# Kernel tuning notes

Measured on AMD Instinct MI355X. Metric: run time of the kernel, lower is better.

## Reference

```python
import jax, jax.numpy as jnp
import numpy as np

NUM_EXPERT = 16
IN_DIM = 1024
OUT_DIM = 3072
TOTAL_TOKENS = 16384  # tokens pre-grouped by expert, contiguous blocks


def setup_inputs() -> dict:
    key = jax.random.key(0)
    k1, k2, k3 = jax.random.split(key, 3)
    inp = jax.random.normal(k1, (TOTAL_TOKENS, IN_DIM), dtype=jnp.float32)
    # per-expert token counts (sum == TOTAL_TOKENS); even split here
    fwd_expert_count = jnp.full((NUM_EXPERT,), TOTAL_TOKENS // NUM_EXPERT, dtype=jnp.int64)
    scale = 1.0 / np.sqrt(IN_DIM)
    weight = jax.random.normal(k2, (NUM_EXPERT, OUT_DIM, IN_DIM), dtype=jnp.float32) * scale
    bias = jax.random.normal(k3, (NUM_EXPERT, OUT_DIM), dtype=jnp.float32) * scale
    return {"inp": inp, "fwd_expert_count": fwd_expert_count, "weight": weight, "bias": bias}


def reference(inp, fwd_expert_count, weight, bias):
    # Grouped GEMM: token block e (size fwd_expert_count[e]) uses expert e's
    # weight: y = x @ W_e^T + b_e.  Tokens are contiguous per expert, so
    # expert id per token = repeat(arange(E), counts).
    T = inp.shape[0]
    E = weight.shape[0]
    expert_id = jnp.repeat(jnp.arange(E), fwd_expert_count, total_repeat_length=T)  # [T]
    out = jnp.zeros((T, weight.shape[1]), dtype=inp.dtype)
    # small fixed structural loop over experts (E=16); each iter is a dense GEMM
    for e in range(E):
        ye = inp @ weight[e].T + bias[e]  # [T, out_dim]
        out = jnp.where((expert_id == e)[:, None], ye, out)
    return out
```

## Files before the change

### kernel.cpp

```cpp
#include <hip/hip_runtime.h>

typedef __attribute__((ext_vector_type(8)))  _Float16 f16x8;
typedef __attribute__((ext_vector_type(2)))  __fp16   fp16x2;
typedef __attribute__((ext_vector_type(4)))  float    f32x4;

#define TT 16384
#define KD 1024
#define ND 3072
#define NE 16
#define ASZ (TT * KD)
#define WSZ (NE * ND * KD)
#define NEED_WS ((size_t)(ASZ + WSZ) * 2)

#define BM 256
#define BN 256
#define BK 64
#define NSTEP (KD / BK)
#define ROWB (BK * 2)

#define BAR() __builtin_amdgcn_s_barrier()
#define WAIT_VM(n) asm volatile("s_waitcnt vmcnt(" #n ")" ::: "memory")

__device__ __forceinline__ int swz(int row, int kbyte) {
    return row * ROWB + (kbyte ^ ((row & 7) << 4));
}

__device__ __forceinline__ int find_expert(const void* cntp, int row0) {
    const int* w = (const int*)cntp;
    int oddsum = 0;
    #pragma unroll
    for (int i = 1; i < 16; i += 2) oddsum |= w[i];
    int e = 0;
    long long cum = 0;
    if (oddsum == 0) {
        const long long* c = (const long long*)cntp;
        #pragma unroll
        for (int i = 0; i < NE; ++i) { if ((long long)row0 >= cum) e = i; cum += c[i]; }
    } else {
        #pragma unroll
        for (int i = 0; i < NE; ++i) { if ((long long)row0 >= cum) e = i; cum += w[i]; }
    }
    return e;
}

__device__ __forceinline__ void gl16(const void* g, void* l) {
    __builtin_amdgcn_global_load_lds(
        (const __attribute__((address_space(1))) unsigned int*)g,
        (__attribute__((address_space(3))) unsigned int*)l, 16, 0, 0);
}

__global__ __launch_bounds__(256) void cvt_kernel(const float* __restrict__ A,
                                                  const float* __restrict__ W,
                                                  _Float16* __restrict__ dst) {
    size_t i = ((size_t)blockIdx.x * 256 + threadIdx.x) * 8;
    const float* src = (i < (size_t)ASZ) ? (A + i) : (W + (i - ASZ));
    f32x4 v0 = *(const f32x4*)src;
    f32x4 v1 = *(const f32x4*)(src + 4);
    f16x8 h;
    h[0] = (_Float16)v0[0]; h[1] = (_Float16)v0[1];
    h[2] = (_Float16)v0[2]; h[3] = (_Float16)v0[3];
    h[4] = (_Float16)v1[0]; h[5] = (_Float16)v1[1];
    h[6] = (_Float16)v1[2]; h[7] = (_Float16)v1[3];
    *(f16x8*)(dst + i) = h;
}

#define MFMA_Q(MH, NH) do {                                                  \
    _Pragma("unroll")                                                        \
    for (int kk = 0; kk < 2; ++kk)                                           \
        _Pragma("unroll")                                                    \
        for (int m = 0; m < 4; ++m)                                          \
            _Pragma("unroll")                                                \
            for (int n = 0; n < 2; ++n)                                      \
                acc[MH][NH][m][n] = __builtin_amdgcn_mfma_f32_16x16x32_f16(  \
                    af[kk][m], bf[kk][n], acc[MH][NH][m][n], 0, 0, 0);       \
} while (0)

__launch_bounds__(512, 2)
__global__ void gemm16(const _Float16* __restrict__ A16,
                       const void* __restrict__ cnt,
                       const _Float16* __restrict__ W16,
                       const float* __restrict__ bias,
                       float* __restrict__ Y) {
    __shared__ __align__(16) char Aslot[2][2][128 * ROWB];
    __shared__ __align__(16) char Bslot[2][2][128 * ROWB];

    const int nwg = gridDim.x;
    const int bid0 = blockIdx.x;
    const int wgid = (bid0 & 7) * (nwg >> 3) + (bid0 >> 3);

    const int mt = wgid / (ND / BN);
    const int nt = wgid % (ND / BN);
    const int row0 = mt * BM;
    const int col0 = nt * BN;

    const int e = find_expert(cnt, row0);
    const _Float16* We = W16 + (size_t)e * ND * KD;

    const int tid = threadIdx.x;
    const int l = tid & 63;
    const int w = tid >> 6;
    const int wr = w >> 2;
    const int wc = w & 3;
    const int lr = l & 15;
    const int lk = l >> 4;

    const int laneoff = ((l & 7) * 16) ^ ((l >> 3) << 4);
    const size_t srcoff = (size_t)(w * 16 + (l >> 3)) * (KD * 2) + laneoff;

    const char* gA0 = (const char*)A16 + (size_t)row0 * (KD * 2);
    const char* gA1 = gA0 + (size_t)128 * (KD * 2);
    const char* gB0 = (const char*)We + (size_t)col0 * (KD * 2);
    const char* gB1 = gB0 + (size_t)128 * (KD * 2);

    auto stage_half = [&](const char* ghalf, char* slot, int t) {
        const char* s = ghalf + t * 128 + srcoff;
        gl16(s,                slot + w * 2048);
        gl16(s + 8 * (KD * 2), slot + w * 2048 + 1024);
    };

    f32x4 acc[2][2][4][2] = {};

    stage_half(gA0, &Aslot[0][0][0], 0);
    stage_half(gB0, &Bslot[0][0][0], 0);
    stage_half(gA1, &Aslot[1][0][0], 0);
    stage_half(gB1, &Bslot[1][0][0], 0);
    stage_half(gA0, &Aslot[0][1][0], 1);
    stage_half(gB0, &Bslot[0][1][0], 1);
    WAIT_VM(4);
    BAR();

    for (int t = 0; t < NSTEP; ++t) {
        const int par = t & 1, nxt = par ^ 1;
        const char* A0s = Aslot[0][par];
        const char* A1s = Aslot[1][par];
        const char* B0s = Bslot[0][par];
        const char* B1s = Bslot[1][par];

        f16x8 af[2][4], bf[2][2];

        auto read_A = [&](const char* slot) {
            #pragma unroll
            for (int kk = 0; kk < 2; ++kk)
                #pragma unroll
                for (int m = 0; m < 4; ++m) {
                    int r = wr * 64 + m * 16 + lr;
                    af[kk][m] = *(const f16x8*)&slot[swz(r, kk * 64 + lk * 16)];
                }
        };
        auto read_B = [&](const char* slot) {
            #pragma unroll
            for (int kk = 0; kk < 2; ++kk)
                #pragma unroll
                for (int n = 0; n < 2; ++n) {
                    int r = wc * 32 + n * 16 + lr;
                    bf[kk][n] = *(const f16x8*)&slot[swz(r, kk * 64 + lk * 16)];
                }
        };

        read_A(A0s);
        read_B(B0s);
        if (t + 1 < NSTEP) {
            stage_half(gA1, &Aslot[1][nxt][0], t + 1);
            stage_half(gB1, &Bslot[1][nxt][0], t + 1);
        }
        BAR();
        __builtin_amdgcn_s_setprio(1);
        MFMA_Q(0, 0);
        __builtin_amdgcn_s_setprio(0);
        BAR();

        read_B(B1s);
        if (t + 2 < NSTEP) stage_half(gA0, &Aslot[0][par][0], t + 2);
        BAR();
        __builtin_amdgcn_s_setprio(1);
        MFMA_Q(0, 1);
        __builtin_amdgcn_s_setprio(0);
        BAR();

        read_A(A1s);
        read_B(B0s);
        BAR();
        __builtin_amdgcn_s_setprio(1);
        MFMA_Q(1, 0);
        __builtin_amdgcn_s_setprio(0);
        BAR();

        read_B(B1s);
        if (t + 2 < NSTEP) stage_half(gB0, &Bslot[0][par][0], t + 2);
        BAR();
        __builtin_amdgcn_s_setprio(1);
        MFMA_Q(1, 1);
        __builtin_amdgcn_s_setprio(0);
        if (t + 2 < NSTEP) { WAIT_VM(4); }
        else if (t + 1 < NSTEP) { WAIT_VM(0); }
        BAR();
    }

    float bv[2][2];
    #pragma unroll
    for (int nh = 0; nh < 2; ++nh)
        #pragma unroll
        for (int n = 0; n < 2; ++n)
            bv[nh][n] = bias[(size_t)e * ND + col0 + nh * 128 + wc * 32 + n * 16 + lr];
    #pragma unroll
    for (int mh = 0; mh < 2; ++mh)
        #pragma unroll
        for (int nh = 0; nh < 2; ++nh)
            #pragma unroll
            for (int m = 0; m < 4; ++m)
                #pragma unroll
                for (int j = 0; j < 4; ++j) {
                    int r = row0 + mh * 128 + wr * 64 + m * 16 + lk * 4 + j;
                    float* yp = Y + (size_t)r * ND + col0 + nh * 128 + wc * 32 + lr;
                    yp[0]  = acc[mh][nh][m][0][j] + bv[nh][0];
                    yp[16] = acc[mh][nh][m][1][j] + bv[nh][1];
                }
}

__launch_bounds__(512, 2)
__global__ void fallback_gemm(const float* __restrict__ A,
                              const void* __restrict__ cnt,
                              const float* __restrict__ W,
                              const float* __restrict__ bias,
                              float* __restrict__ Y) {
    __shared__ __align__(16) char ldsbuf[2][2][BM * ROWB];

    const int nwg = gridDim.x;
    const int bid0 = blockIdx.x;
    const int wgid = (bid0 & 7) * (nwg >> 3) + (bid0 >> 3);

    const int mt = wgid / (ND / BN);
    const int nt = wgid % (ND / BN);
    const int row0 = mt * BM;
    const int col0 = nt * BN;

    const int e = find_expert(cnt, row0);
    const float* We = W + (size_t)e * ND * KD;

    const int tid = threadIdx.x;
    const int lane = tid & 63;
    const int w = tid >> 6;
    const int wr = w >> 2;
    const int wc = w & 3;
    const int lr = lane & 15;
    const int lk = lane >> 4;

    int soff[4];
    size_t aoff[4], boff[4];
    #pragma unroll
    for (int c = 0; c < 4; ++c) {
        int q = c * 512 + tid;
        int r = q >> 3;
        int kb = (q & 7) * 8;
        soff[c] = swz(r, kb * 2);
        aoff[c] = (size_t)(row0 + r) * KD + kb;
        boff[c] = (size_t)(col0 + r) * KD + kb;
    }

    f32x4 ra[4][2], rb[4][2];

    auto load_regs = [&](int ks) {
        const int k0 = ks * BK;
        #pragma unroll
        for (int c = 0; c < 4; ++c) {
            const float* ap = A + aoff[c] + k0;
            ra[c][0] = *(const f32x4*)ap;
            ra[c][1] = *(const f32x4*)(ap + 4);
            const float* bp = We + boff[c] + k0;
            rb[c][0] = *(const f32x4*)bp;
            rb[c][1] = *(const f32x4*)(bp + 4);
        }
    };

    auto write_lds = [&](int buf) {
        #pragma unroll
        for (int c = 0; c < 4; ++c) {
            union { f16x8 v; fp16x2 h[4]; } ua, ub;
            ua.h[0] = __builtin_amdgcn_cvt_pkrtz(ra[c][0][0], ra[c][0][1]);
            ua.h[1] = __builtin_amdgcn_cvt_pkrtz(ra[c][0][2], ra[c][0][3]);
            ua.h[2] = __builtin_amdgcn_cvt_pkrtz(ra[c][1][0], ra[c][1][1]);
            ua.h[3] = __builtin_amdgcn_cvt_pkrtz(ra[c][1][2], ra[c][1][3]);
            ub.h[0] = __builtin_amdgcn_cvt_pkrtz(rb[c][0][0], rb[c][0][1]);
            ub.h[1] = __builtin_amdgcn_cvt_pkrtz(rb[c][0][2], rb[c][0][3]);
            ub.h[2] = __builtin_amdgcn_cvt_pkrtz(rb[c][1][0], rb[c][1][1]);
            ub.h[3] = __builtin_amdgcn_cvt_pkrtz(rb[c][1][2], rb[c][1][3]);
            *(f16x8*)&ldsbuf[buf][0][soff[c]] = ua.v;
            *(f16x8*)&ldsbuf[buf][1][soff[c]] = ub.v;
        }
    };

    f32x4 acc[8][4] = {};

    auto compute = [&](const char* Asb, const char* Bsb) {
        #pragma unroll
        for (int kk = 0; kk < 2; ++kk) {
            f16x8 af[8], bf[4];
            #pragma unroll
            for (int m = 0; m < 8; ++m) {
                int r = wr * 128 + m * 16 + lr;
                af[m] = *(const f16x8*)&Asb[swz(r, kk * 64 + lk * 16)];
            }
            #pragma unroll
            for (int n = 0; n < 4; ++n) {
                int r = wc * 64 + n * 16 + lr;
                bf[n] = *(const f16x8*)&Bsb[swz(r, kk * 64 + lk * 16)];
            }
            #pragma unroll
            for (int m = 0; m < 8; ++m)
                #pragma unroll
                for (int n = 0; n < 4; ++n)
                    acc[m][n] = __builtin_amdgcn_mfma_f32_16x16x32_f16(
                        af[m], bf[n], acc[m][n], 0, 0, 0);
        }
    };

    load_regs(0);
    write_lds(0);
    __syncthreads();

    for (int t = 0; t < NSTEP; ++t) {
        const int buf = t & 1;
        if (t + 1 < NSTEP) load_regs(t + 1);
        compute(ldsbuf[buf][0], ldsbuf[buf][1]);
        __syncthreads();
        if (t + 1 < NSTEP) write_lds(buf ^ 1);
        __syncthreads();
    }

    const int cb = col0 + wc * 64;
    const int rb0_ = row0 + wr * 128;
    float bv[4];
    #pragma unroll
    for (int n = 0; n < 4; ++n) bv[n] = bias[(size_t)e * ND + cb + n * 16 + lr];
    #pragma unroll
    for (int m = 0; m < 8; ++m) {
        #pragma unroll
        for (int j = 0; j < 4; ++j) {
            int r = rb0_ + m * 16 + lk * 4 + j;
            float* yp = Y + (size_t)r * ND + cb + lr;
            #pragma unroll
            for (int n = 0; n < 4; ++n)
                yp[n * 16] = acc[m][n][j] + bv[n];
        }
    }
}

extern "C" void kernel_launch(void* const* d_in, const int* in_sizes, int n_in,
                              void* d_out, int out_size, void* d_ws, size_t ws_size,
                              hipStream_t stream) {
    const float* inp  = (const float*)d_in[0];
    const void*  cnt  = d_in[1];
    const float* wgt  = (const float*)d_in[2];
    const float* bias = (const float*)d_in[3];
    float* out = (float*)d_out;

    dim3 grid((TT / BM) * (ND / BN));
    dim3 block(512);

    if (ws_size >= NEED_WS) {
        _Float16* ws16 = (_Float16*)d_ws;
        cvt_kernel<<<dim3((ASZ + WSZ) / (8 * 256)), dim3(256), 0, stream>>>(inp, wgt, ws16);
        gemm16<<<grid, block, 0, stream>>>(ws16, cnt, ws16 + ASZ, bias, out);
    } else {
        fallback_gemm<<<grid, block, 0, stream>>>(inp, cnt, wgt, bias, out);
    }
}
```

Measured before the change: 224.0 us.

## Restructure GEMM main loop with register fragment reuse and fewer barriers

Result: faster. 197.0 us (-12.0%).

```diff
diff --git a/kernel.cpp b/kernel.cpp
--- a/kernel.cpp
+++ b/kernel.cpp
@@ -64,7 +64,8 @@
     *(f16x8*)(dst + i) = h;
 }
 
-#define MFMA_Q(MH, NH) do {                                                  \
+#define MFMA16(AF, BF, MH, NH) do {                                          \
+    __builtin_amdgcn_s_setprio(1);                                           \
     _Pragma("unroll")                                                        \
     for (int kk = 0; kk < 2; ++kk)                                           \
         _Pragma("unroll")                                                    \
@@ -72,7 +73,8 @@
             _Pragma("unroll")                                                \
             for (int n = 0; n < 2; ++n)                                      \
                 acc[MH][NH][m][n] = __builtin_amdgcn_mfma_f32_16x16x32_f16(  \
-                    af[kk][m], bf[kk][n], acc[MH][NH][m][n], 0, 0, 0);       \
+                    AF[kk][m], BF[kk][n], acc[MH][NH][m][n], 0, 0, 0);       \
+    __builtin_amdgcn_s_setprio(0);                                           \
 } while (0)
 
 __launch_bounds__(512, 2)
@@ -119,81 +121,69 @@
     };
 
     f32x4 acc[2][2][4][2] = {};
+    f16x8 af0[2][4], af1[2][4], bf0[2][2], bf1[2][2];
+
+    auto read_A = [&](f16x8 (&af)[2][4], const char* slot) {
+        #pragma unroll
+        for (int kk = 0; kk < 2; ++kk)
+            #pragma unroll
+            for (int m = 0; m < 4; ++m) {
+                int r = wr * 64 + m * 16 + lr;
+                af[kk][m] = *(const f16x8*)&slot[swz(r, kk * 64 + lk * 16)];
+            }
+    };
+    auto read_B = [&](f16x8 (&bf)[2][2], const char* slot) {
+        #pragma unroll
+        for (int kk = 0; kk < 2; ++kk)
+            #pragma unroll
+            for (int n = 0; n < 2; ++n) {
+                int r = wc * 32 + n * 16 + lr;
+                bf[kk][n] = *(const f16x8*)&slot[swz(r, kk * 64 + lk * 16)];
+            }
+    };
 
     stage_half(gA0, &Aslot[0][0][0], 0);
     stage_half(gB0, &Bslot[0][0][0], 0);
     stage_half(gA1, &Aslot[1][0][0], 0);
     stage_half(gB1, &Bslot[1][0][0], 0);
-    stage_half(gA0, &Aslot[0][1][0], 1);
-    stage_half(gB0, &Bslot[0][1][0], 1);
-    WAIT_VM(4);
-    BAR();
-
-    for (int t = 0; t < NSTEP; ++t) {
+
+    for (int t = 0; t < NSTEP - 1; ++t) {
         const int par = t & 1, nxt = par ^ 1;
-        const char* A0s = Aslot[0][par];
-        const char* A1s = Aslot[1][par];
-        const char* B0s = Bslot[0][par];
-        const char* B1s = Bslot[1][par];
-
-        f16x8 af[2][4], bf[2][2];
-
-        auto read_A = [&](const char* slot) {
-            #pragma unroll
-            for (int kk = 0; kk < 2; ++kk)
-                #pragma unroll
-                for (int m = 0; m < 4; ++m) {
-                    int r = wr * 64 + m * 16 + lr;
-                    af[kk][m] = *(const f16x8*)&slot[swz(r, kk * 64 + lk * 16)];
-                }
-        };
-        auto read_B = [&](const char* slot) {
-            #pragma unroll
-            for (int kk = 0; kk < 2; ++kk)
-                #pragma unroll
-                for (int n = 0; n < 2; ++n) {
-                    int r = wc * 32 + n * 16 + lr;
-                    bf[kk][n] = *(const f16x8*)&slot[swz(r, kk * 64 + lk * 16)];
-                }
-        };
-
-        read_A(A0s);
-        read_B(B0s);
-        if (t + 1 < NSTEP) {
-            stage_half(gA1, &Aslot[1][nxt][0], t + 1);
-            stage_half(gB1, &Bslot[1][nxt][0], t + 1);
-        }
-        BAR();
-        __builtin_amdgcn_s_setprio(1);
-        MFMA_Q(0, 0);
-        __builtin_amdgcn_s_setprio(0);
-        BAR();
-
-        read_B(B1s);
-        if (t + 2 < NSTEP) stage_half(gA0, &Aslot[0][par][0], t + 2);
-        BAR();
-        __builtin_amdgcn_s_setprio(1);
-        MFMA_Q(0, 1);
-        __builtin_amdgcn_s_setprio(0);
-        BAR();
-
-        read_A(A1s);
-        read_B(B0s);
-        BAR();
-        __builtin_amdgcn_s_setprio(1);
-        MFMA_Q(1, 0);
-        __builtin_amdgcn_s_setprio(0);
-        BAR();
-
-        read_B(B1s);
-        if (t + 2 < NSTEP) stage_half(gB0, &Bslot[0][par][0], t + 2);
-        BAR();
-        __builtin_amdgcn_s_setprio(1);
-        MFMA_Q(1, 1);
-        __builtin_amdgcn_s_setprio(0);
-        if (t + 2 < NSTEP) { WAIT_VM(4); }
-        else if (t + 1 < NSTEP) { WAIT_VM(0); }
-        BAR();
+        WAIT_VM(4);
+        BAR();
+        read_A(af0, Aslot[0][par]);
+        read_B(bf0, Bslot[0][par]);
+        stage_half(gA0, &Aslot[0][nxt][0], t + 1);
+        MFMA16(af0, bf0, 0, 0);
+        WAIT_VM(4);
+        BAR();
+        read_A(af1, Aslot[1][par]);
+        stage_half(gB0, &Bslot[0][nxt][0], t + 1);
+        MFMA16(af1, bf0, 1, 0);
+        WAIT_VM(4);
+        BAR();
+        read_B(bf1, Bslot[1][par]);
+        stage_half(gA1, &Aslot[1][nxt][0], t + 1);
+        MFMA16(af1, bf1, 1, 1);
+        stage_half(gB1, &Bslot[1][nxt][0], t + 1);
+        MFMA16(af0, bf1, 0, 1);
+    }
+    {
+        const int par = (NSTEP - 1) & 1;
+        WAIT_VM(4);
+        BAR();
+        read_A(af0, Aslot[0][par]);
+        read_B(bf0, Bslot[0][par]);
+        MFMA16(af0, bf0, 0, 0);
+        WAIT_VM(2);
+        BAR();
+        read_A(af1, Aslot[1][par]);
+        MFMA16(af1, bf0, 1, 0);
+        WAIT_VM(0);
+        BAR();
+        read_B(bf1, Bslot[1][par]);
+        MFMA16(af1, bf1, 1, 1);
+        MFMA16(af0, bf1, 0, 1);
     }
 
     float bv[2][2];
```
